# Kernel tuning notes

Measured on AMD Instinct MI355X. Metric: run time of the kernel, lower is better.

The kernel has to match this reference:

```python
import jax, jax.numpy as jnp
import numpy as np

B, D, N, K = 16, 128, 4096, 1024


def setup_inputs() -> dict:
    key = jax.random.key(0)
    k1, k2 = jax.random.split(key)
    ze = jax.random.normal(k1, (B, D, N), dtype=jnp.float32)
    emb = jax.random.normal(k2, (K, D), dtype=jnp.float32)
    return {"ze": ze, "emb": emb}


def reference(ze, emb):
    """VQ forward: nearest-codebook quantization with straight-through estimator.

    ze:  (B, D, N) encoder latents (D = n_latent_dim, N = timesteps)
    emb: (K, D) codebook (stop-gradient applied, matching StopGrad on emb)
    returns zq_rg: (B, D, N) quantized latents; gradient flows straight to ze
    (ReplaceGrad: zq gets zero grad, ze gets the output grad).
    """
    emb_sg = jax.lax.stop_gradient(emb)
    # Squared L2 distance via expansion, avoiding the (B, D, K, N) broadcast:
    # d2[b,k,n] = ||ze[b,:,n]||^2 + ||emb[k]||^2 - 2 <ze[b,:,n], emb[k]>
    ze_sq = jnp.sum(ze * ze, axis=1)            # (B, N)
    emb_sq = jnp.sum(emb_sg * emb_sg, axis=1)   # (K,)
    dot = jnp.einsum('bdn,kd->bkn', ze, emb_sg)  # (B, K, N)
    d2 = ze_sq[:, None, :] + emb_sq[None, :, None] - 2.0 * dot
    ind = jnp.argmin(d2, axis=1)                # (B, N) nearest codebook index
    zq = jnp.transpose(jnp.take(emb_sg, ind, axis=0), (0, 2, 1))  # (B, D, N)
    # ReplaceGrad straight-through: value of zq, gradient routed to ze.
    zq_rg = ze + jax.lax.stop_gradient(zq - ze)
    return zq_rg
```

## Files before the change

### kernel.cpp

```cpp
#include <hip/hip_runtime.h>
#include <hip/hip_bf16.h>
#include <math.h>

#define BB 16
#define DD 128
#define NN 4096
#define KK 1024
#define CADD 320.0f
#define TAU 0.45f

typedef __attribute__((ext_vector_type(8))) short short8;
typedef __attribute__((ext_vector_type(4))) float f32x4;

static __device__ __forceinline__ unsigned short f32_bf16_rne(float f) {
    unsigned u = __float_as_uint(f);
    u += 0x7FFF + ((u >> 16) & 1);
    return (unsigned short)(u >> 16);
}
static __device__ __forceinline__ unsigned umin32(unsigned a, unsigned b) { return a < b ? a : b; }
static __device__ __forceinline__ unsigned umax32(unsigned a, unsigned b) { return a > b ? a : b; }
static __device__ __forceinline__ unsigned umed3(unsigned a, unsigned b, unsigned c) {
    unsigned d;
    asm("v_med3_u32 %0, %1, %2, %3" : "=v"(d) : "v"(a), "v"(b), "v"(c));
    return d;
}

__global__ void emb_sq_kernel(const float* __restrict__ emb,
                              float* __restrict__ e2) {
    int k = blockIdx.x * 256 + threadIdx.x;
    if (k >= KK) return;
    const float4* row = reinterpret_cast<const float4*>(emb + (size_t)k * DD);
    float a0 = 0.f, a1 = 0.f, a2 = 0.f, a3 = 0.f;
#pragma unroll
    for (int i = 0; i < DD / 16; ++i) {
        float4 v0 = row[i * 4 + 0];
        float4 v1 = row[i * 4 + 1];
        float4 v2 = row[i * 4 + 2];
        float4 v3 = row[i * 4 + 3];
        a0 += v0.x * v0.x + v0.y * v0.y + v0.z * v0.z + v0.w * v0.w;
        a1 += v1.x * v1.x + v1.y * v1.y + v1.z * v1.z + v1.w * v1.w;
        a2 += v2.x * v2.x + v2.y * v2.y + v2.z * v2.z + v2.w * v2.w;
        a3 += v3.x * v3.x + v3.y * v3.y + v3.z * v3.z + v3.w * v3.w;
    }
    e2[k] = (a0 + a1) + (a2 + a3) + CADD;
}

__global__ void emb_pack_kernel(const float* __restrict__ emb,
                                short* __restrict__ epk) {
    int g = blockIdx.x * 256 + threadIdx.x;
    int lane = g & 63;
    int s    = (g >> 6) & 3;
    int t    = g >> 8;
    int k = t * 16 + (lane & 15);
    int d = s * 32 + ((lane >> 4) & 3) * 8;
    const float* src = emb + (size_t)k * DD + d;
    short8 h;
#pragma unroll
    for (int j = 0; j < 8; ++j) h[j] = (short)f32_bf16_rne(-2.0f * src[j]);
    *reinterpret_cast<short8*>(epk + (size_t)g * 8) = h;
}

#define CEU(a, b) { unsigned lo_ = umin32(a, b), hi_ = umax32(a, b); (a) = lo_; (b) = hi_; }
#define MRG9(A1, A2, A3, A4, B1, B2, B3, B4) \
    CEU(A1, B1) CEU(A2, B2) CEU(A3, B3) CEU(A4, B4) \
    CEU(A3, B1) CEU(A4, B2) \
    CEU(A2, A3) \
    CEU(A4, B1) \
    CEU(A3, A4)

__global__ __launch_bounds__(256, 4)
void vq_mfma(const float* __restrict__ ze, const float* __restrict__ emb,
             const short* __restrict__ epk, const float* __restrict__ e2,
             float* __restrict__ out) {
    __shared__ __align__(16) char ubuf[(DD + 1) * 64 * 4];
    __shared__ unsigned kbuf[4][64][4];
    __shared__ int winner_s[64];
    __shared__ int rlist[64];
    __shared__ int rcnt;

    short* zstage = reinterpret_cast<short*>(ubuf);

    const int tid  = threadIdx.x;
    const int lane = tid & 63;
    const int wave = tid >> 6;
    const int b    = blockIdx.x >> 6;
    const int n0b  = (blockIdx.x & 63) * 64;
    const float* zb = ze + (size_t)b * DD * NN;

    const int nq = lane & 15;
    const int dq = (lane >> 4) & 3;

#pragma unroll
    for (int cg = 0; cg < 4; ++cg) {
        const int col = n0b + cg * 16 + nq;
        const int d0  = wave * 32 + dq * 8;
        const float* zp = zb + (size_t)d0 * NN + col;
        short8 h;
#pragma unroll
        for (int j = 0; j < 8; ++j) h[j] = (short)f32_bf16_rne(zp[(size_t)j * NN]);
        *reinterpret_cast<short8*>(zstage + (cg * 256 + wave * 64 + lane) * 8) = h;
    }
    __syncthreads();

    short8 zf[4][4];
#pragma unroll
    for (int cg = 0; cg < 4; ++cg)
#pragma unroll
        for (int s = 0; s < 4; ++s)
            zf[cg][s] = *reinterpret_cast<const short8*>(
                zstage + ((cg * 4 + s) * 64 + lane) * 8);
    __syncthreads();

    unsigned K1[4], K2[4];
#pragma unroll
    for (int cg = 0; cg < 4; ++cg) { K1[cg] = K2[cg] = 0xFFFFFFFFu; }

    const int t0 = wave * 16;
    const short* ep  = epk + (size_t)(t0 * 4) * 512 + (size_t)lane * 8;
    const float* e2p = e2 + t0 * 16 + dq * 4;
    unsigned kb = (unsigned)(t0 * 16 + dq * 4);

#pragma unroll 2
    for (int tt = 0; tt < 16; ++tt) {
        const short8 a0 = *reinterpret_cast<const short8*>(ep);
        const short8 a1 = *reinterpret_cast<const short8*>(ep + 512);
        const short8 a2 = *reinterpret_cast<const short8*>(ep + 1024);
        const short8 a3 = *reinterpret_cast<const short8*>(ep + 1536);
        const float4 ev = *reinterpret_cast<const float4*>(e2p);

        f32x4 acc0 = {ev.x, ev.y, ev.z, ev.w};
        f32x4 acc1 = acc0, acc2 = acc0, acc3 = acc0;
#define STEP(AF, S) \
        acc0 = __builtin_amdgcn_mfma_f32_16x16x32_bf16(AF, zf[0][S], acc0, 0, 0, 0); \
        acc1 = __builtin_amdgcn_mfma_f32_16x16x32_bf16(AF, zf[1][S], acc1, 0, 0, 0); \
        acc2 = __builtin_amdgcn_mfma_f32_16x16x32_bf16(AF, zf[2][S], acc2, 0, 0, 0); \
        acc3 = __builtin_amdgcn_mfma_f32_16x16x32_bf16(AF, zf[3][S], acc3, 0, 0, 0);
        STEP(a0, 0) STEP(a1, 1) STEP(a2, 2) STEP(a3, 3)
#undef STEP

#pragma unroll
        for (int cg = 0; cg < 4; ++cg) {
            const f32x4 a = (cg == 0) ? acc0 : (cg == 1) ? acc1
                          : (cg == 2) ? acc2 : acc3;
#pragma unroll
            for (int r = 0; r < 4; ++r) {
                const unsigned x = (__float_as_uint(a[r]) & 0xFFFFFC00u) | (kb + r);
                K2[cg] = umed3(K1[cg], K2[cg], x);
                K1[cg] = umin32(K1[cg], x);
            }
        }
        kb += 16; ep += 2048; e2p += 16;
    }

    unsigned T1[4], T2[4], T3[4], T4[4];
#pragma unroll
    for (int cg = 0; cg < 4; ++cg) {
        unsigned A1 = K1[cg], A2 = K2[cg];
        unsigned B1 = __shfl_xor(A1, 16);
        unsigned B2 = __shfl_xor(A2, 16);
        CEU(A1, B1) CEU(A2, B2) CEU(A2, B1)
        unsigned C1 = __shfl_xor(A1, 32);
        unsigned C2 = __shfl_xor(A2, 32);
        unsigned C3 = __shfl_xor(B1, 32);
        unsigned C4 = __shfl_xor(B2, 32);
        MRG9(A1, A2, B1, B2, C1, C2, C3, C4)
        T1[cg] = A1; T2[cg] = A2; T3[cg] = B1; T4[cg] = B2;
    }

    {
        const int cgid = lane >> 4;
#define SEL4(T) ((cgid & 2) ? ((cgid & 1) ? T[3] : T[2]) : ((cgid & 1) ? T[1] : T[0]))
        kbuf[wave][lane][0] = SEL4(T1);
        kbuf[wave][lane][1] = SEL4(T2);
        kbuf[wave][lane][2] = SEL4(T3);
        kbuf[wave][lane][3] = SEL4(T4);
#undef SEL4
    }
    __syncthreads();

    if (wave == 0) {
        const int c = lane;
        unsigned A1 = kbuf[0][c][0], A2 = kbuf[0][c][1];
        unsigned A3 = kbuf[0][c][2], A4 = kbuf[0][c][3];
#pragma unroll
        for (int q = 1; q < 4; ++q) {
            unsigned B1 = kbuf[q][c][0], B2 = kbuf[q][c][1];
            unsigned B3 = kbuf[q][c][2], B4 = kbuf[q][c][3];
            MRG9(A1, A2, A3, A4, B1, B2, B3, B4)
        }
        const float M1 = __uint_as_float(A1 & 0xFFFFFC00u);
        const float M2 = __uint_as_float(A2 & 0xFFFFFC00u);
        const bool trig = (M2 - M1) < TAU;
        winner_s[c] = (int)(A1 & 0x3FFu);
        kbuf[0][c][0] = A1; kbuf[0][c][1] = A2;
        kbuf[0][c][2] = A3; kbuf[0][c][3] = A4;
        const unsigned long long mask = __ballot(trig);
        if (trig) {
            const int idx = __popcll(mask & ((1ull << lane) - 1ull));
            rlist[idx] = c;
        }
        if (lane == 0) rcnt = (int)__popcll(mask);
    }
    __syncthreads();

    {
        const int rc = rcnt;
        for (int j = wave; j < rc; j += 4) {
            const int c = rlist[j];
            const int coln = n0b + c;
            const int I0 = (int)(kbuf[0][c][0] & 0x3FFu);
            const int I1 = (int)(kbuf[0][c][1] & 0x3FFu);
            const int I2 = (int)(kbuf[0][c][2] & 0x3FFu);
            const int I3 = (int)(kbuf[0][c][3] & 0x3FFu);
            double s0 = 0.0, s1 = 0.0, s2 = 0.0, s3 = 0.0;
#pragma unroll
            for (int h = 0; h < 2; ++h) {
                const int d = h * 64 + lane;
                const double zv = (double)zb[(size_t)d * NN + coln];
                double q;
                q = zv - (double)emb[(size_t)I0 * DD + d]; s0 += q * q;
                q = zv - (double)emb[(size_t)I1 * DD + d]; s1 += q * q;
                q = zv - (double)emb[(size_t)I2 * DD + d]; s2 += q * q;
                q = zv - (double)emb[(size_t)I3 * DD + d]; s3 += q * q;
            }
#pragma unroll
            for (int off = 1; off < 64; off <<= 1) {
                s0 += __shfl_xor(s0, off);
                s1 += __shfl_xor(s1, off);
                s2 += __shfl_xor(s2, off);
                s3 += __shfl_xor(s3, off);
            }
            int best = I0; double db = s0;
            if (s1 < db || (s1 == db && I1 < best)) { db = s1; best = I1; }
            if (s2 < db || (s2 == db && I2 < best)) { db = s2; best = I2; }
            if (s3 < db || (s3 == db && I3 < best)) { db = s3; best = I3; }
            if (lane == 0) winner_s[c] = best;
        }
    }
    __syncthreads();

    float (*ew)[DD + 1] = reinterpret_cast<float(*)[DD + 1]>(ubuf);
#pragma unroll 4
    for (int rr = 0; rr < 16; ++rr) {
        const int r = wave * 16 + rr;
        const int idx = winner_s[r];
        ew[r][lane]      = emb[(size_t)idx * DD + lane];
        ew[r][lane + 64] = emb[(size_t)idx * DD + lane + 64];
    }
    __syncthreads();

    {
        const int coln = n0b + lane;
#pragma unroll 4
        for (int dd = 0; dd < 32; ++dd) {
            const int d = wave * 32 + dd;
            const float zv = zb[(size_t)d * NN + coln];
            const float evv = ew[lane][d];
            out[((size_t)b * DD + d) * NN + coln] = zv + (evv - zv);
        }
    }
}

extern "C" void kernel_launch(void* const* d_in, const int* in_sizes, int n_in,
                              void* d_out, int out_size, void* d_ws, size_t ws_size,
                              hipStream_t stream) {
    (void)in_sizes; (void)n_in; (void)out_size; (void)ws_size;
    const float* ze  = (const float*)d_in[0];
    const float* emb = (const float*)d_in[1];
    float*       out = (float*)d_out;

    char* ws = (char*)d_ws;
    short* epk = (short*)ws;
    float* e2  = (float*)(ws + (size_t)KK * DD * 2);

    emb_sq_kernel<<<KK / 256, 256, 0, stream>>>(emb, e2);
    emb_pack_kernel<<<(KK * DD / 8) / 256, 256, 0, stream>>>(emb, epk);
    vq_mfma<<<(BB * NN) / 64, 256, 0, stream>>>(ze, emb, epk, e2, out);
}
```

Before: 45.29 us.

## Double block column tile to 128 with 8 waves sharing codebook loads

Each block now handles 128 columns with 512 threads. Wave pairs split the column halves while four K-quarters are spread across waves, so each codebook fragment loaded from global memory feeds twice as many columns. The refinement and output stages are reorganised for 128 columns, and the embedding gather now runs in two 64-dim passes to fit shared memory. The trade-offs are half as many blocks (1024 → 512), extra barriers, and higher shared-memory and register pressure per block under launch_bounds(512,4).

After: 46.02 us. Within noise of the previous version (+1.6%).

```diff
diff --git a/kernel.cpp b/kernel.cpp
--- a/kernel.cpp
+++ b/kernel.cpp
@@ -68,54 +68,57 @@
     CEU(A4, B1) \
     CEU(A3, A4)
 
-__global__ __launch_bounds__(256, 4)
+__global__ __launch_bounds__(512, 4)
 void vq_mfma(const float* __restrict__ ze, const float* __restrict__ emb,
              const short* __restrict__ epk, const float* __restrict__ e2,
              float* __restrict__ out) {
-    __shared__ __align__(16) char ubuf[(DD + 1) * 64 * 4];
-    __shared__ unsigned kbuf[4][64][4];
-    __shared__ int winner_s[64];
-    __shared__ int rlist[64];
-    __shared__ int rcnt;
+    __shared__ __align__(16) char ubuf[128 * 65 * 4];
+    __shared__ unsigned kbuf[4][128][4];
+    __shared__ int winner_s[128];
+    __shared__ int rlist[128];
+    __shared__ int rcnt0, rcnt1;
 
     short* zstage = reinterpret_cast<short*>(ubuf);
 
     const int tid  = threadIdx.x;
     const int lane = tid & 63;
     const int wave = tid >> 6;
-    const int b    = blockIdx.x >> 6;
-    const int n0b  = (blockIdx.x & 63) * 64;
+    const int colhalf = wave & 1;
+    const int kq      = wave >> 1;
+    const int b    = blockIdx.x >> 5;
+    const int n0b  = (blockIdx.x & 31) * 128;
     const float* zb = ze + (size_t)b * DD * NN;
 
     const int nq = lane & 15;
     const int dq = (lane >> 4) & 3;
 
 #pragma unroll
-    for (int cg = 0; cg < 4; ++cg) {
+    for (int c4 = 0; c4 < 4; ++c4) {
+        const int cg  = (wave >> 2) * 4 + c4;
         const int col = n0b + cg * 16 + nq;
-        const int d0  = wave * 32 + dq * 8;
+        const int d0  = (wave & 3) * 32 + dq * 8;
         const float* zp = zb + (size_t)d0 * NN + col;
         short8 h;
 #pragma unroll
         for (int j = 0; j < 8; ++j) h[j] = (short)f32_bf16_rne(zp[(size_t)j * NN]);
-        *reinterpret_cast<short8*>(zstage + (cg * 256 + wave * 64 + lane) * 8) = h;
+        *reinterpret_cast<short8*>(zstage + ((cg * 4 + (wave & 3)) * 64 + lane) * 8) = h;
     }
     __syncthreads();
 
     short8 zf[4][4];
 #pragma unroll
-    for (int cg = 0; cg < 4; ++cg)
+    for (int cgp = 0; cgp < 4; ++cgp)
 #pragma unroll
         for (int s = 0; s < 4; ++s)
-            zf[cg][s] = *reinterpret_cast<const short8*>(
-                zstage + ((cg * 4 + s) * 64 + lane) * 8);
+            zf[cgp][s] = *reinterpret_cast<const short8*>(
+                zstage + (((colhalf * 4 + cgp) * 4 + s) * 64 + lane) * 8);
     __syncthreads();
 
     unsigned K1[4], K2[4];
 #pragma unroll
     for (int cg = 0; cg < 4; ++cg) { K1[cg] = K2[cg] = 0xFFFFFFFFu; }
 
-    const int t0 = wave * 16;
+    const int t0 = kq * 16;
     const short* ep  = epk + (size_t)(t0 * 4) * 512 + (size_t)lane * 8;
     const float* e2p = e2 + t0 * 16 + dq * 4;
     unsigned kb = (unsigned)(t0 * 16 + dq * 4);
@@ -169,17 +172,18 @@
 
     {
         const int cgid = lane >> 4;
+        const int c = colhalf * 64 + lane;
 #define SEL4(T) ((cgid & 2) ? ((cgid & 1) ? T[3] : T[2]) : ((cgid & 1) ? T[1] : T[0]))
-        kbuf[wave][lane][0] = SEL4(T1);
-        kbuf[wave][lane][1] = SEL4(T2);
-        kbuf[wave][lane][2] = SEL4(T3);
-        kbuf[wave][lane][3] = SEL4(T4);
+        kbuf[kq][c][0] = SEL4(T1);
+        kbuf[kq][c][1] = SEL4(T2);
+        kbuf[kq][c][2] = SEL4(T3);
+        kbuf[kq][c][3] = SEL4(T4);
 #undef SEL4
     }
     __syncthreads();
 
-    if (wave == 0) {
-        const int c = lane;
+    if (wave < 2) {
+        const int c = wave * 64 + lane;
         unsigned A1 = kbuf[0][c][0], A2 = kbuf[0][c][1];
         unsigned A3 = kbuf[0][c][2], A4 = kbuf[0][c][3];
 #pragma unroll
@@ -197,67 +201,81 @@
         const unsigned long long mask = __ballot(trig);
         if (trig) {
             const int idx = __popcll(mask & ((1ull << lane) - 1ull));
-            rlist[idx] = c;
-        }
-        if (lane == 0) rcnt = (int)__popcll(mask);
+            rlist[wave * 64 + idx] = c;
+        }
+        if (lane == 0) {
+            if (wave == 0) rcnt0 = (int)__popcll(mask);
+            else           rcnt1 = (int)__popcll(mask);
+        }
     }
     __syncthreads();
 
     {
-        const int rc = rcnt;
-        for (int j = wave; j < rc; j += 4) {
-            const int c = rlist[j];
+        const int rc0 = rcnt0, rc1 = rcnt1;
+#pragma unroll 1
+        for (int seg = 0; seg < 2; ++seg) {
+            const int rc = seg ? rc1 : rc0;
+            const int base = seg * 64;
+            for (int j = wave; j < rc; j += 8) {
+                const int c = rlist[base + j];
+                const int coln = n0b + c;
+                const int I0 = (int)(kbuf[0][c][0] & 0x3FFu);
+                const int I1 = (int)(kbuf[0][c][1] & 0x3FFu);
+                const int I2 = (int)(kbuf[0][c][2] & 0x3FFu);
+                const int I3 = (int)(kbuf[0][c][3] & 0x3FFu);
+                double s0 = 0.0, s1 = 0.0, s2 = 0.0, s3 = 0.0;
+#pragma unroll
+                for (int h = 0; h < 2; ++h) {
+                    const int d = h * 64 + lane;
+                    const double zv = (double)zb[(size_t)d * NN + coln];
+                    double q;
+                    q = zv - (double)emb[(size_t)I0 * DD + d]; s0 += q * q;
+                    q = zv - (double)emb[(size_t)I1 * DD + d]; s1 += q * q;
+                    q = zv - (double)emb[(size_t)I2 * DD + d]; s2 += q * q;
+                    q = zv - (double)emb[(size_t)I3 * DD + d]; s3 += q * q;
+                }
+#pragma unroll
+                for (int off = 1; off < 64; off <<= 1) {
+                    s0 += __shfl_xor(s0, off);
+                    s1 += __shfl_xor(s1, off);
+                    s2 += __shfl_xor(s2, off);
+                    s3 += __shfl_xor(s3, off);
+                }
+                int best = I0; double db = s0;
+                if (s1 < db || (s1 == db && I1 < best)) { db = s1; best = I1; }
+                if (s2 < db || (s2 == db && I2 < best)) { db = s2; best = I2; }
+                if (s3 < db || (s3 == db && I3 < best)) { db = s3; best = I3; }
+                if (lane == 0) winner_s[c] = best;
+            }
+        }
+    }
+    __syncthreads();
+
+    float (*ew)[65] = reinterpret_cast<float(*)[65]>(ubuf);
+#pragma unroll 1
+    for (int pass = 0; pass < 2; ++pass) {
+        const int dbase = pass * 64;
+#pragma unroll 4
+        for (int rr = 0; rr < 16; ++rr) {
+            const int r = wave * 16 + rr;
+            const int idx = winner_s[r];
+            ew[r][lane] = emb[(size_t)idx * DD + dbase + lane];
+        }
+        __syncthreads();
+        {
+            const int c = tid & 127;
+            const int dgrp = tid >> 7;
             const int coln = n0b + c;
-            const int I0 = (int)(kbuf[0][c][0] & 0x3FFu);
-            const int I1 = (int)(kbuf[0][c][1] & 0x3FFu);
-            const int I2 = (int)(kbuf[0][c][2] & 0x3FFu);
-            const int I3 = (int)(kbuf[0][c][3] & 0x3FFu);
-            double s0 = 0.0, s1 = 0.0, s2 = 0.0, s3 = 0.0;
-#pragma unroll
-            for (int h = 0; h < 2; ++h) {
-                const int d = h * 64 + lane;
-                const double zv = (double)zb[(size_t)d * NN + coln];
-                double q;
-                q = zv - (double)emb[(size_t)I0 * DD + d]; s0 += q * q;
-                q = zv - (double)emb[(size_t)I1 * DD + d]; s1 += q * q;
-                q = zv - (double)emb[(size_t)I2 * DD + d]; s2 += q * q;
-                q = zv - (double)emb[(size_t)I3 * DD + d]; s3 += q * q;
+#pragma unroll 4
+            for (int dd = 0; dd < 16; ++dd) {
+                const int dl = dd * 4 + dgrp;
+                const int d  = dbase + dl;
+                const float zv  = zb[(size_t)d * NN + coln];
+                const float evv = ew[c][dl];
+                out[((size_t)b * DD + d) * NN + coln] = zv + (evv - zv);
             }
-#pragma unroll
-            for (int off = 1; off < 64; off <<= 1) {
-                s0 += __shfl_xor(s0, off);
-                s1 += __shfl_xor(s1, off);
-                s2 += __shfl_xor(s2, off);
-                s3 += __shfl_xor(s3, off);
-            }
-            int best = I0; double db = s0;
-            if (s1 < db || (s1 == db && I1 < best)) { db = s1; best = I1; }
-            if (s2 < db || (s2 == db && I2 < best)) { db = s2; best = I2; }
-            if (s3 < db || (s3 == db && I3 < best)) { db = s3; best = I3; }
-            if (lane == 0) winner_s[c] = best;
-        }
-    }
-    __syncthreads();
-
-    float (*ew)[DD + 1] = reinterpret_cast<float(*)[DD + 1]>(ubuf);
-#pragma unroll 4
-    for (int rr = 0; rr < 16; ++rr) {
-        const int r = wave * 16 + rr;
-        const int idx = winner_s[r];
-        ew[r][lane]      = emb[(size_t)idx * DD + lane];
-        ew[r][lane + 64] = emb[(size_t)idx * DD + lane + 64];
-    }
-    __syncthreads();
-
-    {
-        const int coln = n0b + lane;
-#pragma unroll 4
-        for (int dd = 0; dd < 32; ++dd) {
-            const int d = wave * 32 + dd;
-            const float zv = zb[(size_t)d * NN + coln];
-            const float evv = ew[lane][d];
-            out[((size_t)b * DD + d) * NN + coln] = zv + (evv - zv);
-        }
+        }
+        __syncthreads();
     }
 }
 
@@ -275,5 +293,5 @@
 
     emb_sq_kernel<<<KK / 256, 256, 0, stream>>>(emb, e2);
     emb_pack_kernel<<<(KK * DD / 8) / 256, 256, 0, stream>>>(emb, epk);
-    vq_mfma<<<(BB * NN) / 64, 256, 0, stream>>>(ze, emb, epk, e2, out);
-}
+    vq_mfma<<<(BB * NN) / 128, 512, 0, stream>>>(ze, emb, epk, e2, out);
+}
```
